# Kernel optimization log

Measured on AMD Instinct MI355X. Metric: run time of the kernel, lower is better.

## Reference

```python
import jax, jax.numpy as jnp
import numpy as np

DIM = 1024
K = 9            # kernel_size
PAD = 4          # padding = (K-1)//2


def setup_inputs() -> dict:
    key = jax.random.key(0)
    k1, k2, k3, k4, k5 = jax.random.split(key, 5)
    b, l, d = 4, 4096, DIM
    s = 1.0 / np.sqrt(d)
    x = jax.random.normal(k1, (b, l, d), dtype=jnp.float32)
    # linear2: dim -> k^2 + k   (torch Linear: y = x @ W.T + b)
    w2 = jax.random.uniform(k2, (K * K + K, d), jnp.float32, -s, s)
    b2 = jax.random.uniform(k3, (K * K + K,), jnp.float32, -s, s)
    # outlinear: dim -> dim
    wo = jax.random.uniform(k4, (d, d), jnp.float32, -s, s)
    bo = jax.random.uniform(k5, (d,), jnp.float32, -s, s)
    return {"x": x, "w2": w2, "b2": b2, "wo": wo, "bo": bo}


def reference(x, w2, b2, wo, bo):
    b, l, d = x.shape
    # per-token generated weights / bias
    att = x @ w2.T + b2                                  # (b, l, k^2 + k)
    aw = jnp.sin(att[..., : K * K]).reshape(b, l, K, K)  # (b, l, k, k)
    ab = att[..., K * K :]                               # (b, l, k)
    # sliding windows along sequence: (b, l, d, k)
    xp = jnp.pad(x, ((0, 0), (PAD, PAD), (0, 0)))
    windows = jnp.stack([xp[:, i : i + l] for i in range(K)], axis=-1)
    # sum_j (windows @ aw)[..., j] == windows @ aw.sum(-1); bias sums over k, broadcast over d
    y = jnp.einsum("bldk,blk->bld", windows, aw.sum(axis=-1)) + ab.sum(axis=-1, keepdims=True)
    return y @ wo.T + bo
```

## Files before the change

### kernel.cpp

```cpp
#include <hip/hip_runtime.h>
#include <hip/hip_bf16.h>

#define DIM   1024
#define SEQL  4096
#define NTOK  16384
#define NATT  90
#define NATTP 96

typedef __attribute__((ext_vector_type(8))) short frag_ab;
typedef __attribute__((ext_vector_type(4))) float frag_cd;

typedef unsigned int u32;
typedef const __attribute__((address_space(1))) u32* gp_t;
typedef __attribute__((address_space(3))) u32* lp_t;

static __device__ __forceinline__ unsigned short f2bf(float f) {
    unsigned int u = __float_as_uint(f);
    return (unsigned short)((u + 0x7fffu + ((u >> 16) & 1u)) >> 16);
}
static __device__ __forceinline__ ushort4 f4tobf(float4 v) {
    ushort4 r; r.x = f2bf(v.x); r.y = f2bf(v.y); r.z = f2bf(v.z); r.w = f2bf(v.w);
    return r;
}
static __device__ __forceinline__ float4 bf4tof(ushort4 u) {
    float4 r;
    r.x = __uint_as_float((u32)u.x << 16);
    r.y = __uint_as_float((u32)u.y << 16);
    r.z = __uint_as_float((u32)u.z << 16);
    r.w = __uint_as_float((u32)u.w << 16);
    return r;
}

__global__ __launch_bounds__(256) void cvt_w2_kernel(
    const float* __restrict__ w2, unsigned short* __restrict__ w2p)
{
    const int idx = blockIdx.x * 256 + threadIdx.x;
    const int c    = idx / 384;
    const int rem  = idx - c * 384;
    const int f    = rem >> 6;
    const int lane = rem & 63;
    const int row  = f * 16 + (lane & 15);
    const int col  = c * 32 + (lane >> 4) * 8;
    float4 v0 = make_float4(0.f, 0.f, 0.f, 0.f), v1 = v0;
    if (row < NATT) {
        v0 = *(const float4*)(w2 + (size_t)row * DIM + col);
        v1 = *(const float4*)(w2 + (size_t)row * DIM + col + 4);
    }
    unsigned short* dst = w2p + (size_t)idx * 8;
    *(ushort4*)(dst)     = f4tobf(v0);
    *(ushort4*)(dst + 4) = f4tobf(v1);
}

#define ATOK 16
#define PSTR 98

__global__ __launch_bounds__(256) void att_y_kernel(
    const float* __restrict__ x, const unsigned short* __restrict__ w2p,
    const float* __restrict__ b2, const float* __restrict__ wo,
    unsigned short* __restrict__ ybf, unsigned short* __restrict__ wob)
{
    __shared__ __align__(16) unsigned short xs[ATOK * 1024];
    __shared__ float part[ATOK * PSTR];
    __shared__ float b2s[NATTP];
    __shared__ float coe[ATOK][12];

    const int tid  = threadIdx.x;
    const int bid = blockIdx.x;

    if (bid >= 1024) {
        const int i = (bid - 1024) * 256 + tid;
        float4 v = ((const float4*)wo)[i];
        *(ushort4*)(wob + (size_t)i * 4) = f4tobf(v);
        return;
    }

    const int wave = tid >> 6, lane = tid & 63;
    const int fr = lane & 15, kq = lane >> 4;
    const int lid = (bid & 7) * 128 + (bid >> 3);
    const int tok0 = lid * ATOK;
    const int bb = tok0 >> 12;
    const int l0 = tok0 & 4095;

    if (tid < NATTP) b2s[tid] = (tid < NATT) ? b2[tid] : 0.f;

    #pragma unroll
    for (int t = 0; t < 4; ++t) {
        const int row = t * 4 + wave;
        const float4* xr = (const float4*)(x + (size_t)(tok0 + row) * DIM);
        #pragma unroll
        for (int tt = 0; tt < 4; ++tt) {
            const int c4 = tt * 64 + lane;
            float4 v = xr[c4];
            const int ch = c4 >> 1, half = c4 & 1;
            *(ushort4*)(&xs[row * 1024 + ((ch ^ (row & 7)) * 8 + half * 4)]) = f4tobf(v);
        }
    }

    const float4 z4 = make_float4(0.f, 0.f, 0.f, 0.f);
    float4 halo[8];
    #pragma unroll
    for (int hh = 0; hh < 8; ++hh) {
        const int off = (hh < 4) ? (hh - 4) : (hh + 12);
        const int src = l0 + off;
        halo[hh] = z4;
        if (src >= 0 && src < SEQL)
            halo[hh] = *((const float4*)(x + ((size_t)bb * SEQL + src) * DIM) + tid);
    }
    __syncthreads();

    const int fbase = (wave & 1) * 3;
    const int kh    = wave >> 1;
    frag_cd acc[3] = {};
    #pragma unroll
    for (int kk = 0; kk < 16; ++kk) {
        const int ch = kh * 64 + kk * 4 + kq;
        frag_ab a = *(const frag_ab*)(&xs[fr * 1024 + ((ch ^ (fr & 7)) * 8)]);
        const int c = kh * 16 + kk;
        #pragma unroll
        for (int ff = 0; ff < 3; ++ff) {
            const int f = fbase + ff;
            frag_ab b = *(const frag_ab*)(w2p + ((size_t)((c * 6 + f) * 64) + lane) * 8);
            acc[ff] = __builtin_amdgcn_mfma_f32_16x16x32_bf16(a, b, acc[ff], 0, 0, 0);
        }
    }

    const int col = lane & 15, rb = (lane >> 4) * 4;
    if (kh == 0) {
        #pragma unroll
        for (int ff = 0; ff < 3; ++ff)
            #pragma unroll
            for (int r = 0; r < 4; ++r)
                part[(rb + r) * PSTR + (fbase + ff) * 16 + col]
                    = acc[ff][r] + b2s[(fbase + ff) * 16 + col];
    }
    __syncthreads();
    if (kh == 1) {
        #pragma unroll
        for (int ff = 0; ff < 3; ++ff)
            #pragma unroll
            for (int r = 0; r < 4; ++r)
                part[(rb + r) * PSTR + (fbase + ff) * 16 + col] += acc[ff][r];
    }
    __syncthreads();

    if (tid < 160) {
        const int t = tid / 10, j = tid - (tid / 10) * 10;
        float s = 0.f;
        if (j < 9) {
            #pragma unroll
            for (int jj = 0; jj < 9; ++jj) s += sinf(part[t * PSTR + j * 9 + jj]);
        } else {
            #pragma unroll
            for (int m = NATT - 9; m < NATT; ++m) s += part[t * PSTR + m];
        }
        coe[t][j] = s;
    }
    __syncthreads();

    const int ch2 = tid >> 1, hf2 = tid & 1;
    auto rowval = [&](int rel) -> float4 {
        if (rel < 0)  return halo[rel + 4];
        if (rel > 15) return halo[rel - 12];
        ushort4 u = *(const ushort4*)(&xs[rel * 1024 + ((ch2 ^ (rel & 7)) * 8 + hf2 * 4)]);
        return bf4tof(u);
    };

    float4 w[9];
    #pragma unroll
    for (int k = 0; k < 8; ++k) w[k] = rowval(k - 4);

    #pragma unroll
    for (int t = 0; t < ATOK; ++t) {
        w[8] = rowval(t + 4);
        float4 a4;
        a4.x = a4.y = a4.z = a4.w = coe[t][9];
        #pragma unroll
        for (int k = 0; k < 9; ++k) {
            const float ck = coe[t][k];
            a4.x += ck * w[k].x; a4.y += ck * w[k].y;
            a4.z += ck * w[k].z; a4.w += ck * w[k].w;
        }
        *(ushort4*)(ybf + (size_t)(tok0 + t) * DIM + tid * 4) = f4tobf(a4);
        #pragma unroll
        for (int k = 0; k < 8; ++k) w[k] = w[k + 1];
    }
}

#define GBM 256
#define GBN 256
#define GBK 64

#define STAGE(d, kt)                                                           \
    {                                                                          \
        const int kc_ = (kt) * GBK;                                            \
        _Pragma("unroll")                                                      \
        for (int j_ = 0; j_ < 4; ++j_) {                                       \
            __builtin_amdgcn_global_load_lds(                                  \
                (gp_t)(A + (size_t)(m0 + srow[j_]) * DIM + kc_ + scol[j_]),    \
                (lp_t)(&As[d][(wave * 4 + j_) * 512]), 16, 0, 0);              \
            __builtin_amdgcn_global_load_lds(                                  \
                (gp_t)(Bm + (size_t)(n0 + srow[j_]) * DIM + kc_ + scol[j_]),   \
                (lp_t)(&Bs[d][(wave * 4 + j_) * 512]), 16, 0, 0);              \
        }                                                                      \
    }

__global__ __launch_bounds__(512, 2) void gemm_kernel(
    const unsigned short* __restrict__ A,
    const unsigned short* __restrict__ Bm,
    const float* __restrict__ bo,
    float* __restrict__ out)
{
    __shared__ unsigned short As[2][GBM * GBK];
    __shared__ unsigned short Bs[2][GBN * GBK];

    const int tid  = threadIdx.x;
    const int wave = tid >> 6, lane = tid & 63;
    const int fr = lane & 15, kq = lane >> 4;
    const int wm = (wave >> 2) * 128;
    const int wn = (wave & 3) * 64;

    const int bid = blockIdx.x;
    const int lid = (bid & 7) * 32 + (bid >> 3);
    const int m0  = (lid >> 2) * GBM;
    const int n0  = (lid & 3) * GBN;

    int srow[4], scol[4];
    #pragma unroll
    for (int j = 0; j < 4; ++j) {
        int ci = (wave * 4 + j) * 64 + lane;
        int row = ci >> 3;
        srow[j] = row;
        scol[j] = ((ci & 7) ^ (row & 7)) * 8;
    }

    frag_cd acc[8][4] = {};

    STAGE(0, 0);
    STAGE(1, 1);

    for (int kt = 0; kt < 15; ++kt) {
        const int d = kt & 1;
        asm volatile("s_waitcnt vmcnt(8)" ::: "memory");
        __builtin_amdgcn_s_barrier();

        frag_ab b0[4], b1[4];
        #pragma unroll
        for (int ni = 0; ni < 4; ++ni) {
            int row = wn + ni * 16 + fr;
            b0[ni] = *(const frag_ab*)(&Bs[d][row * 64 + ((kq       ^ (row & 7)) * 8)]);
            b1[ni] = *(const frag_ab*)(&Bs[d][row * 64 + (((4 + kq) ^ (row & 7)) * 8)]);
        }
        frag_ab alo0[4], alo1[4];
        #pragma unroll
        for (int mi = 0; mi < 4; ++mi) {
            int row = wm + mi * 16 + fr;
            alo0[mi] = *(const frag_ab*)(&As[d][row * 64 + ((kq       ^ (row & 7)) * 8)]);
            alo1[mi] = *(const frag_ab*)(&As[d][row * 64 + (((4 + kq) ^ (row & 7)) * 8)]);
        }
        __builtin_amdgcn_s_setprio(1);
        #pragma unroll
        for (int mi = 0; mi < 4; ++mi)
            #pragma unroll
            for (int ni = 0; ni < 4; ++ni) {
                acc[mi][ni] = __builtin_amdgcn_mfma_f32_16x16x32_bf16(alo0[mi], b0[ni], acc[mi][ni], 0, 0, 0);
                acc[mi][ni] = __builtin_amdgcn_mfma_f32_16x16x32_bf16(alo1[mi], b1[ni], acc[mi][ni], 0, 0, 0);
            }
        __builtin_amdgcn_s_setprio(0);
        frag_ab ahi0[4], ahi1[4];
        #pragma unroll
        for (int mi = 0; mi < 4; ++mi) {
            int row = wm + (mi + 4) * 16 + fr;
            ahi0[mi] = *(const frag_ab*)(&As[d][row * 64 + ((kq       ^ (row & 7)) * 8)]);
            ahi1[mi] = *(const frag_ab*)(&As[d][row * 64 + (((4 + kq) ^ (row & 7)) * 8)]);
        }
        asm volatile("s_waitcnt lgkmcnt(0)" ::: "memory");
        __builtin_amdgcn_s_barrier();
        if (kt < 14) { STAGE(d, kt + 2); }
        __builtin_amdgcn_s_setprio(1);
        #pragma unroll
        for (int mi = 0; mi < 4; ++mi)
            #pragma unroll
            for (int ni = 0; ni < 4; ++ni) {
                acc[mi + 4][ni] = __builtin_amdgcn_mfma_f32_16x16x32_bf16(ahi0[mi], b0[ni], acc[mi + 4][ni], 0, 0, 0);
                acc[mi + 4][ni] = __builtin_amdgcn_mfma_f32_16x16x32_bf16(ahi1[mi], b1[ni], acc[mi + 4][ni], 0, 0, 0);
            }
        __builtin_amdgcn_s_setprio(0);
    }

    {
        asm volatile("s_waitcnt vmcnt(0)" ::: "memory");
        __builtin_amdgcn_s_barrier();
        frag_ab b0[4], b1[4];
        #pragma unroll
        for (int ni = 0; ni < 4; ++ni) {
            int row = wn + ni * 16 + fr;
            b0[ni] = *(const frag_ab*)(&Bs[1][row * 64 + ((kq       ^ (row & 7)) * 8)]);
            b1[ni] = *(const frag_ab*)(&Bs[1][row * 64 + (((4 + kq) ^ (row & 7)) * 8)]);
        }
        #pragma unroll
        for (int h = 0; h < 2; ++h) {
            frag_ab a0[4], a1[4];
            #pragma unroll
            for (int mi = 0; mi < 4; ++mi) {
                int row = wm + (mi + h * 4) * 16 + fr;
                a0[mi] = *(const frag_ab*)(&As[1][row * 64 + ((kq       ^ (row & 7)) * 8)]);
                a1[mi] = *(const frag_ab*)(&As[1][row * 64 + (((4 + kq) ^ (row & 7)) * 8)]);
            }
            __builtin_amdgcn_s_setprio(1);
            #pragma unroll
            for (int mi = 0; mi < 4; ++mi)
                #pragma unroll
                for (int ni = 0; ni < 4; ++ni) {
                    acc[mi + h * 4][ni] = __builtin_amdgcn_mfma_f32_16x16x32_bf16(a0[mi], b0[ni], acc[mi + h * 4][ni], 0, 0, 0);
                    acc[mi + h * 4][ni] = __builtin_amdgcn_mfma_f32_16x16x32_bf16(a1[mi], b1[ni], acc[mi + h * 4][ni], 0, 0, 0);
                }
            __builtin_amdgcn_s_setprio(0);
        }
    }

    const int colb = lane & 15, rb = (lane >> 4) * 4;
    #pragma unroll
    for (int ni = 0; ni < 4; ++ni) {
        const int col = n0 + wn + ni * 16 + colb;
        const float bias = bo[col];
        #pragma unroll
        for (int mi = 0; mi < 8; ++mi) {
            #pragma unroll
            for (int r = 0; r < 4; ++r) {
                const int row = m0 + wm + mi * 16 + rb + r;
                out[(size_t)row * DIM + col] = acc[mi][ni][r] + bias;
            }
        }
    }
}

extern "C" void kernel_launch(void* const* d_in, const int* in_sizes, int n_in,
                              void* d_out, int out_size, void* d_ws, size_t ws_size,
                              hipStream_t stream) {
    const float* x  = (const float*)d_in[0];
    const float* w2 = (const float*)d_in[1];
    const float* b2 = (const float*)d_in[2];
    const float* wo = (const float*)d_in[3];
    const float* bo = (const float*)d_in[4];
    float* out = (float*)d_out;

    char* ws = (char*)d_ws;
    unsigned short* wob = (unsigned short*)ws;
    unsigned short* ybf = (unsigned short*)(ws + 2097152);
    unsigned short* w2p = (unsigned short*)(ws + 2097152 + 33554432);

    cvt_w2_kernel<<<48, 256, 0, stream>>>(w2, w2p);
    att_y_kernel<<<2048, 256, 0, stream>>>(x, w2p, b2, wo, ybf, wob);
    gemm_kernel<<<NTOK / GBM * (DIM / GBN), 512, 0, stream>>>(ybf, wob, bo, out);
}
```

Baseline: 76.54 us.

## Restructure GEMM main loop into eight-phase half-tile pipeline with interleaved staging

Rewrites the bf16 GEMM mainloop so the LDS tiles are split into 128-row halves and each k-step is broken into four phases. Each phase reads a small A fragment set, issues a slice of the next global-to-LDS loads, then runs its MFMAs, with barriers between phases. The aim is finer-grained overlap of memory traffic with matrix math and lower register pressure from holding fewer A fragments at once. In exchange it adds many more barriers per k-step and a more fragile hand-tuned schedule of waitcnt values.

```diff
diff --git a/kernel.cpp b/kernel.cpp
--- a/kernel.cpp
+++ b/kernel.cpp
@@ -186,23 +186,60 @@
     }
 }
 
-#define GBM 256
-#define GBN 256
-#define GBK 64
-
-#define STAGE(d, kt)                                                           \
-    {                                                                          \
-        const int kc_ = (kt) * GBK;                                            \
-        _Pragma("unroll")                                                      \
-        for (int j_ = 0; j_ < 4; ++j_) {                                       \
-            __builtin_amdgcn_global_load_lds(                                  \
-                (gp_t)(A + (size_t)(m0 + srow[j_]) * DIM + kc_ + scol[j_]),    \
-                (lp_t)(&As[d][(wave * 4 + j_) * 512]), 16, 0, 0);              \
-            __builtin_amdgcn_global_load_lds(                                  \
-                (gp_t)(Bm + (size_t)(n0 + srow[j_]) * DIM + kc_ + scol[j_]),   \
-                (lp_t)(&Bs[d][(wave * 4 + j_) * 512]), 16, 0, 0);              \
-        }                                                                      \
-    }
+
+#define VMC4 asm volatile("s_waitcnt vmcnt(4)" ::: "memory")
+#define VMC0 asm volatile("s_waitcnt vmcnt(0)" ::: "memory")
+#define BAR  __builtin_amdgcn_s_barrier()
+
+#define STG_HALF(Ls, gbase, goff, dd, hh, kt) {                                 \
+    _Pragma("unroll")                                                           \
+    for (int j_ = 0; j_ < 2; ++j_) {                                            \
+        const int ci_ = j_ * 512 + tid;                                         \
+        const int r_ = ci_ >> 3, c_ = ((ci_ & 7) ^ (r_ & 7)) * 8;               \
+        __builtin_amdgcn_global_load_lds(                                       \
+            (gp_t)(gbase + (size_t)((goff) + (hh) * 128 + r_) * DIM             \
+                   + (kt) * 64 + c_),                                           \
+            (lp_t)(&Ls[dd][hh][(j_ * 8 + wave) * 512]), 16, 0, 0);              \
+    } }
+
+#define RD_B_ALL(dd) {                                                          \
+    _Pragma("unroll")                                                           \
+    for (int ni_ = 0; ni_ < 4; ++ni_) {                                         \
+        const int rr_ = (wn & 127) + ni_ * 16 + fr;                             \
+        b0[ni_] = *(const frag_ab*)(&Bs[dd][bh][rr_ * 64 + ((kq       ^ (fr & 7)) * 8)]); \
+        b1[ni_] = *(const frag_ab*)(&Bs[dd][bh][rr_ * 64 + (((4 + kq) ^ (fr & 7)) * 8)]); \
+    } }
+
+#define RD_A2(dd, q) {                                                          \
+    _Pragma("unroll")                                                           \
+    for (int m2_ = 0; m2_ < 2; ++m2_) {                                         \
+        const int rr_ = ((q) * 2 + m2_) * 16 + fr;                              \
+        a0[m2_] = *(const frag_ab*)(&As[dd][ah][rr_ * 64 + ((kq       ^ (fr & 7)) * 8)]); \
+        a1[m2_] = *(const frag_ab*)(&As[dd][ah][rr_ * 64 + (((4 + kq) ^ (fr & 7)) * 8)]); \
+    } }
+
+#define PHASE(dd, q, STG, VM) {                                                 \
+    if ((q) == 0) RD_B_ALL(dd);                                                 \
+    RD_A2(dd, q);                                                               \
+    STG;                                                                        \
+    BAR;                                                                        \
+    __builtin_amdgcn_s_setprio(1);                                              \
+    _Pragma("unroll")                                                           \
+    for (int m2_ = 0; m2_ < 2; ++m2_)                                           \
+        _Pragma("unroll")                                                       \
+        for (int ni_ = 0; ni_ < 4; ++ni_)                                       \
+            acc[(q) * 2 + m2_][ni_] = __builtin_amdgcn_mfma_f32_16x16x32_bf16(  \
+                a0[m2_], b0[ni_], acc[(q) * 2 + m2_][ni_], 0, 0, 0);            \
+    _Pragma("unroll")                                                           \
+    for (int m2_ = 0; m2_ < 2; ++m2_)                                           \
+        _Pragma("unroll")                                                       \
+        for (int ni_ = 0; ni_ < 4; ++ni_)                                       \
+            acc[(q) * 2 + m2_][ni_] = __builtin_amdgcn_mfma_f32_16x16x32_bf16(  \
+                a1[m2_], b1[ni_], acc[(q) * 2 + m2_][ni_], 0, 0, 0);            \
+    __builtin_amdgcn_s_setprio(0);                                              \
+    VM;                                                                         \
+    BAR;                                                                        \
+  }
 
 __global__ __launch_bounds__(512, 2) void gemm_kernel(
     const unsigned short* __restrict__ A,
@@ -210,125 +247,66 @@
     const float* __restrict__ bo,
     float* __restrict__ out)
 {
-    __shared__ unsigned short As[2][GBM * GBK];
-    __shared__ unsigned short Bs[2][GBN * GBK];
+    __shared__ unsigned short As[2][2][128 * 64];
+    __shared__ unsigned short Bs[2][2][128 * 64];
 
     const int tid  = threadIdx.x;
     const int wave = tid >> 6, lane = tid & 63;
     const int fr = lane & 15, kq = lane >> 4;
     const int wm = (wave >> 2) * 128;
     const int wn = (wave & 3) * 64;
+    const int ah = wave >> 2;
+    const int bh = (wave & 3) >> 1;
 
     const int bid = blockIdx.x;
     const int lid = (bid & 7) * 32 + (bid >> 3);
-    const int m0  = (lid >> 2) * GBM;
-    const int n0  = (lid & 3) * GBN;
-
-    int srow[4], scol[4];
-    #pragma unroll
-    for (int j = 0; j < 4; ++j) {
-        int ci = (wave * 4 + j) * 64 + lane;
-        int row = ci >> 3;
-        srow[j] = row;
-        scol[j] = ((ci & 7) ^ (row & 7)) * 8;
-    }
-
+    const int m0  = (lid >> 2) * 256;
+    const int n0  = (lid & 3) * 256;
+
+    frag_ab b0[4], b1[4], a0[2], a1[2];
     frag_cd acc[8][4] = {};
 
-    STAGE(0, 0);
-    STAGE(1, 1);
-
-    for (int kt = 0; kt < 15; ++kt) {
-        const int d = kt & 1;
-        asm volatile("s_waitcnt vmcnt(8)" ::: "memory");
-        __builtin_amdgcn_s_barrier();
-
-        frag_ab b0[4], b1[4];
-        #pragma unroll
-        for (int ni = 0; ni < 4; ++ni) {
-            int row = wn + ni * 16 + fr;
-            b0[ni] = *(const frag_ab*)(&Bs[d][row * 64 + ((kq       ^ (row & 7)) * 8)]);
-            b1[ni] = *(const frag_ab*)(&Bs[d][row * 64 + (((4 + kq) ^ (row & 7)) * 8)]);
-        }
-        frag_ab alo0[4], alo1[4];
-        #pragma unroll
-        for (int mi = 0; mi < 4; ++mi) {
-            int row = wm + mi * 16 + fr;
-            alo0[mi] = *(const frag_ab*)(&As[d][row * 64 + ((kq       ^ (row & 7)) * 8)]);
-            alo1[mi] = *(const frag_ab*)(&As[d][row * 64 + (((4 + kq) ^ (row & 7)) * 8)]);
-        }
-        __builtin_amdgcn_s_setprio(1);
-        #pragma unroll
-        for (int mi = 0; mi < 4; ++mi)
-            #pragma unroll
-            for (int ni = 0; ni < 4; ++ni) {
-                acc[mi][ni] = __builtin_amdgcn_mfma_f32_16x16x32_bf16(alo0[mi], b0[ni], acc[mi][ni], 0, 0, 0);
-                acc[mi][ni] = __builtin_amdgcn_mfma_f32_16x16x32_bf16(alo1[mi], b1[ni], acc[mi][ni], 0, 0, 0);
-            }
-        __builtin_amdgcn_s_setprio(0);
-        frag_ab ahi0[4], ahi1[4];
-        #pragma unroll
-        for (int mi = 0; mi < 4; ++mi) {
-            int row = wm + (mi + 4) * 16 + fr;
-            ahi0[mi] = *(const frag_ab*)(&As[d][row * 64 + ((kq       ^ (row & 7)) * 8)]);
-            ahi1[mi] = *(const frag_ab*)(&As[d][row * 64 + (((4 + kq) ^ (row & 7)) * 8)]);
-        }
-        asm volatile("s_waitcnt lgkmcnt(0)" ::: "memory");
-        __builtin_amdgcn_s_barrier();
-        if (kt < 14) { STAGE(d, kt + 2); }
-        __builtin_amdgcn_s_setprio(1);
-        #pragma unroll
-        for (int mi = 0; mi < 4; ++mi)
-            #pragma unroll
-            for (int ni = 0; ni < 4; ++ni) {
-                acc[mi + 4][ni] = __builtin_amdgcn_mfma_f32_16x16x32_bf16(ahi0[mi], b0[ni], acc[mi + 4][ni], 0, 0, 0);
-                acc[mi + 4][ni] = __builtin_amdgcn_mfma_f32_16x16x32_bf16(ahi1[mi], b1[ni], acc[mi + 4][ni], 0, 0, 0);
-            }
-        __builtin_amdgcn_s_setprio(0);
-    }
-
-    {
-        asm volatile("s_waitcnt vmcnt(0)" ::: "memory");
-        __builtin_amdgcn_s_barrier();
-        frag_ab b0[4], b1[4];
-        #pragma unroll
-        for (int ni = 0; ni < 4; ++ni) {
-            int row = wn + ni * 16 + fr;
-            b0[ni] = *(const frag_ab*)(&Bs[1][row * 64 + ((kq       ^ (row & 7)) * 8)]);
-            b1[ni] = *(const frag_ab*)(&Bs[1][row * 64 + (((4 + kq) ^ (row & 7)) * 8)]);
-        }
-        #pragma unroll
-        for (int h = 0; h < 2; ++h) {
-            frag_ab a0[4], a1[4];
-            #pragma unroll
-            for (int mi = 0; mi < 4; ++mi) {
-                int row = wm + (mi + h * 4) * 16 + fr;
-                a0[mi] = *(const frag_ab*)(&As[1][row * 64 + ((kq       ^ (row & 7)) * 8)]);
-                a1[mi] = *(const frag_ab*)(&As[1][row * 64 + (((4 + kq) ^ (row & 7)) * 8)]);
-            }
-            __builtin_amdgcn_s_setprio(1);
-            #pragma unroll
-            for (int mi = 0; mi < 4; ++mi)
-                #pragma unroll
-                for (int ni = 0; ni < 4; ++ni) {
-                    acc[mi + h * 4][ni] = __builtin_amdgcn_mfma_f32_16x16x32_bf16(a0[mi], b0[ni], acc[mi + h * 4][ni], 0, 0, 0);
-                    acc[mi + h * 4][ni] = __builtin_amdgcn_mfma_f32_16x16x32_bf16(a1[mi], b1[ni], acc[mi + h * 4][ni], 0, 0, 0);
-                }
-            __builtin_amdgcn_s_setprio(0);
-        }
-    }
+    STG_HALF(Bs, Bm, n0, 0, 0, 0);
+    STG_HALF(Bs, Bm, n0, 0, 1, 0);
+    STG_HALF(As, A,  m0, 0, 0, 0);
+    STG_HALF(As, A,  m0, 0, 1, 0);
+    STG_HALF(Bs, Bm, n0, 1, 0, 1);
+    STG_HALF(Bs, Bm, n0, 1, 1, 1);
+    VMC4;
+    BAR;
+
+    #pragma unroll 1
+    for (int it = 0; it < 7; ++it) {
+        const int T0 = 2 * it, T1 = 2 * it + 1;
+        PHASE(0, 0, { STG_HALF(As, A, m0, 1, 0, T1); STG_HALF(As, A, m0, 1, 1, T1); }, );
+        PHASE(0, 1, { STG_HALF(Bs, Bm, n0, 0, 0, T0 + 2); }, );
+        PHASE(0, 2, { STG_HALF(Bs, Bm, n0, 0, 1, T0 + 2); }, );
+        PHASE(0, 3, , VMC4);
+        PHASE(1, 0, { STG_HALF(As, A, m0, 0, 0, T0 + 2); }, );
+        PHASE(1, 1, { STG_HALF(As, A, m0, 0, 1, T0 + 2); }, );
+        PHASE(1, 2, { STG_HALF(Bs, Bm, n0, 1, 0, T1 + 2); }, );
+        PHASE(1, 3, { STG_HALF(Bs, Bm, n0, 1, 1, T1 + 2); }, VMC4);
+    }
+    PHASE(0, 0, { STG_HALF(As, A, m0, 1, 0, 15); STG_HALF(As, A, m0, 1, 1, 15); }, );
+    PHASE(0, 1, , );
+    PHASE(0, 2, , );
+    PHASE(0, 3, , VMC0);
+    PHASE(1, 0, , );
+    PHASE(1, 1, , );
+    PHASE(1, 2, , );
+    PHASE(1, 3, , );
 
     const int colb = lane & 15, rb = (lane >> 4) * 4;
     #pragma unroll
     for (int ni = 0; ni < 4; ++ni) {
-        const int col = n0 + wn + ni * 16 + colb;
-        const float bias = bo[col];
+        const int colo = n0 + wn + ni * 16 + colb;
+        const float bias = bo[colo];
         #pragma unroll
         for (int mi = 0; mi < 8; ++mi) {
             #pragma unroll
             for (int r = 0; r < 4; ++r) {
-                const int row = m0 + wm + mi * 16 + rb + r;
-                out[(size_t)row * DIM + col] = acc[mi][ni][r] + bias;
+                const int rowo = m0 + wm + mi * 16 + rb + r;
+                out[(size_t)rowo * DIM + colo] = acc[mi][ni][r] + bias;
             }
         }
     }
@@ -351,5 +329,5 @@
 
     cvt_w2_kernel<<<48, 256, 0, stream>>>(w2, w2p);
     att_y_kernel<<<2048, 256, 0, stream>>>(x, w2p, b2, wo, ybf, wob);
-    gemm_kernel<<<NTOK / GBM * (DIM / GBN), 512, 0, stream>>>(ybf, wob, bo, out);
-}
+    gemm_kernel<<<256, 512, 0, stream>>>(ybf, wob, bo, out);
+}
```

Result: no change. 77.23 us (+0.9%).
